# Kernel tuning notes

Measured on AMD Instinct MI355X. Metric: run time of the kernel, lower is better.

The kernel has to match this reference:

```python
import jax, jax.numpy as jnp
import numpy as np

MODES = (16, 16)

def setup_inputs() -> dict:
    key = jax.random.key(0)
    ks = jax.random.split(key, 8)
    B, Cin, Cout, H, W = 16, 64, 64, 128, 128
    scale = 1.0 / (Cin * Cout)
    return {
        "x": jax.random.normal(ks[0], (B, Cin, H, W), jnp.float32),
        "t_emb": jax.random.normal(ks[1], (B, 512), jnp.float32),
        "weight_real": jax.random.normal(ks[2], (Cin, Cout, *MODES), jnp.float32) * 2 * scale - scale,
        "weight_imag": jax.random.normal(ks[3], (Cin, Cout, *MODES), jnp.float32) * 2 * scale - scale,
        "bypass_w": jax.random.normal(ks[4], (Cout, Cin), jnp.float32) * 0.05,
        "bypass_b": jax.random.normal(ks[5], (Cout,), jnp.float32) * 0.05,
        "temb_w": jax.random.normal(ks[6], (Cin, 512), jnp.float32) * 0.02,
        "temb_b": jax.random.normal(ks[7], (Cin,), jnp.float32) * 0.02,
    }

def reference(x, t_emb, weight_real, weight_imag, bypass_w, bypass_b, temb_w, temb_b):
    mk, ml = MODES
    H, W = x.shape[-2:]
    xf = x.astype(jnp.float32)
    # truncated spectral conv: rfft2 (ortho), keep low-mode corner only
    x_fft = jnp.fft.rfftn(xf, axes=(-2, -1), norm="ortho")[:, :, :mk, :ml]
    weight = weight_real + 1j * weight_imag  # [i, o, k, l]
    out_fft = jnp.einsum("bikl,iokl->bokl", x_fft, weight)
    x_spec = jnp.fft.irfftn(out_fft, s=(H, W), axes=(-2, -1), norm="ortho")
    # 1x1 conv bypass
    byp = jnp.einsum("bihw,oi->bohw", xf, bypass_w) + bypass_b[None, :, None, None]
    out = jax.nn.gelu(x_spec + byp, approximate=False)
    # temb fusion: x + Linear(silu(temb))[:, :, None, None]
    silu_t = t_emb * jax.nn.sigmoid(t_emb)
    proj = silu_t @ temb_w.T + temb_b  # [B, C]
    out = out + proj[:, :, None, None]
    return out
```

## Files before the change

kernel.cpp:

```cpp
#include <hip/hip_runtime.h>
#include <cmath>

#define TWO_PI_128 0.04908738521234052f

typedef __attribute__((ext_vector_type(8))) short bf16x8;
typedef __attribute__((ext_vector_type(4))) float f32x4;

__device__ inline unsigned short f2bf(float v) {
  unsigned u = __float_as_uint(v);
  unsigned r = (u + 0x7FFFu + ((u >> 16) & 1u)) >> 16;
  return (unsigned short)r;
}

__global__ __launch_bounds__(256) void proj_kernel(
    const float* __restrict__ t_emb, const float* __restrict__ temb_w,
    const float* __restrict__ temb_b, float* __restrict__ proj) {
  __shared__ float s_silu[512];
  __shared__ float s_part[64][4];
  const int b = blockIdx.x;
  const int t = threadIdx.x;
  for (int j = t; j < 512; j += 256) {
    float v = t_emb[b * 512 + j];
    s_silu[j] = v / (1.f + __expf(-v));
  }
  __syncthreads();
  const int o = t >> 2, part = t & 3;
  const float* wrow = temb_w + o * 512 + part * 128;
  const float* srow = s_silu + part * 128;
  float acc = 0.f;
#pragma unroll 8
  for (int j = 0; j < 128; ++j) acc = fmaf(srow[j], wrow[j], acc);
  s_part[o][part] = acc;
  __syncthreads();
  if (part == 0) {
    proj[b * 64 + o] =
        s_part[o][0] + s_part[o][1] + s_part[o][2] + s_part[o][3] + temb_b[o];
  }
}

__global__ __launch_bounds__(256) void wtrans_kernel(
    const float* __restrict__ wr, const float* __restrict__ wi,
    float* __restrict__ wt_r, float* __restrict__ wt_i) {
  __shared__ float tile[32][33];
  const float* src = blockIdx.z ? wi : wr;
  float* dst = blockIdx.z ? wt_i : wt_r;
  const int kl0 = blockIdx.x * 32, io0 = blockIdx.y * 32;
  const int ty = threadIdx.x >> 3, tx = threadIdx.x & 7;
  float4 v = *(const float4*)(src + (size_t)(io0 + ty) * 256 + kl0 + 4 * tx);
  tile[ty][4 * tx + 0] = v.x;
  tile[ty][4 * tx + 1] = v.y;
  tile[ty][4 * tx + 2] = v.z;
  tile[ty][4 * tx + 3] = v.w;
  __syncthreads();
  float4 o;
  o.x = tile[4 * tx + 0][ty];
  o.y = tile[4 * tx + 1][ty];
  o.z = tile[4 * tx + 2][ty];
  o.w = tile[4 * tx + 3][ty];
  *(float4*)(dst + (size_t)(kl0 + ty) * 4096 + io0 + 4 * tx) = o;
}

__global__ __launch_bounds__(256) void fwd_dft_kernel(
    const float* __restrict__ x, float* __restrict__ xfr_t,
    float* __restrict__ xfi_t) {
  __shared__ unsigned short s_x1[32 * 136];
  __shared__ float s_red[8 * 256];
  const int t = threadIdx.x;
  const int plane = blockIdx.x;
  const int wv = t >> 6, lane = t & 63, l15 = lane & 15, quad = lane >> 4;

  union U8 {
    bf16x8 v;
    unsigned short u[8];
  };

  float dC, dS;
  sincosf(TWO_PI_128 * (float)l15, &dS, &dC);

  U8 a_re[4], a_im[4];
#pragma unroll
  for (int ks = 0; ks < 4; ++ks) {
    const int w0 = ks * 32 + quad * 8;
    float c, s;
    sincosf(TWO_PI_128 * (float)((l15 * w0) & 127), &s, &c);
#pragma unroll
    for (int j = 0; j < 8; ++j) {
      a_re[ks].u[j] = f2bf(c);
      a_im[ks].u[j] = f2bf(-s);
      float nc = c * dC - s * dS;
      s = s * dC + c * dS;
      c = nc;
    }
  }

  const float* xp = x + (size_t)plane * 16384;
  f32x4 acc[2][2];
#pragma unroll
  for (int mt = 0; mt < 2; ++mt)
#pragma unroll
    for (int nt = 0; nt < 2; ++nt) acc[mt][nt] = (f32x4){0.f, 0.f, 0.f, 0.f};

#pragma unroll
  for (int ks = 0; ks < 4; ++ks) {
#pragma unroll
    for (int nt = 0; nt < 2; ++nt) {
      const float* src =
          xp + (size_t)((wv * 2 + nt) * 16 + l15) * 128 + ks * 32 + quad * 8;
      float4 v0 = *(const float4*)src;
      float4 v1 = *(const float4*)(src + 4);
      U8 bx;
      bx.u[0] = f2bf(v0.x);
      bx.u[1] = f2bf(v0.y);
      bx.u[2] = f2bf(v0.z);
      bx.u[3] = f2bf(v0.w);
      bx.u[4] = f2bf(v1.x);
      bx.u[5] = f2bf(v1.y);
      bx.u[6] = f2bf(v1.z);
      bx.u[7] = f2bf(v1.w);
      acc[0][nt] = __builtin_amdgcn_mfma_f32_16x16x32_bf16(a_re[ks].v, bx.v,
                                                           acc[0][nt], 0, 0, 0);
      acc[1][nt] = __builtin_amdgcn_mfma_f32_16x16x32_bf16(a_im[ks].v, bx.v,
                                                           acc[1][nt], 0, 0, 0);
    }
  }

#pragma unroll
  for (int mt = 0; mt < 2; ++mt)
#pragma unroll
    for (int nt = 0; nt < 2; ++nt)
#pragma unroll
      for (int r = 0; r < 4; ++r)
        s_x1[(mt * 16 + quad * 4 + r) * 136 + (wv * 2 + nt) * 16 + l15] =
            f2bf(acc[mt][nt][r]);
  __syncthreads();

  f32x4 accre = (f32x4){0.f, 0.f, 0.f, 0.f};
  f32x4 accim = (f32x4){0.f, 0.f, 0.f, 0.f};
#pragma unroll
  for (int kl2 = 0; kl2 < 2; ++kl2) {
    const int ks2 = wv * 2 + kl2;
    const int hb = (ks2 & 3) * 32 + quad * 8;
    const int imh = ks2 >> 2;
    float c, s;
    sincosf(TWO_PI_128 * (float)((l15 * hb) & 127), &s, &c);
    U8 ar, ai;
#pragma unroll
    for (int j = 0; j < 8; ++j) {
      if (!imh) {
        ar.u[j] = f2bf(c);
        ai.u[j] = f2bf(-s);
      } else {
        ar.u[j] = f2bf(s);
        ai.u[j] = f2bf(c);
      }
      float nc = c * dC - s * dS;
      s = s * dC + c * dS;
      c = nc;
    }
    bf16x8 bfrag = *(const bf16x8*)(s_x1 + (imh * 16 + l15) * 136 + hb);
    accre =
        __builtin_amdgcn_mfma_f32_16x16x32_bf16(ar.v, bfrag, accre, 0, 0, 0);
    accim =
        __builtin_amdgcn_mfma_f32_16x16x32_bf16(ai.v, bfrag, accim, 0, 0, 0);
  }
  *(f32x4*)(s_red + (wv * 2) * 256 + lane * 4) = accre;
  *(f32x4*)(s_red + (wv * 2 + 1) * 256 + lane * 4) = accim;
  __syncthreads();

  const float re = s_red[t] + s_red[512 + t] + s_red[1024 + t] + s_red[1536 + t];
  const float im =
      s_red[256 + t] + s_red[768 + t] + s_red[1280 + t] + s_red[1792 + t];
  const int k = (t >> 6) * 4 + (t & 3), l = (t >> 2) & 15;
  xfr_t[(size_t)(k * 16 + l) * 1024 + plane] = re * 0.0078125f;
  xfi_t[(size_t)(k * 16 + l) * 1024 + plane] = im * 0.0078125f;
}

__global__ __launch_bounds__(256) void modemix_kernel(
    const float* __restrict__ xfr_t, const float* __restrict__ xfi_t,
    const float* __restrict__ wt_r, const float* __restrict__ wt_i,
    float* __restrict__ ofr, float* __restrict__ ofi) {
  __shared__ float s_xr[1024], s_xi[1024];
  __shared__ float s_wr[4096], s_wi[4096];
  const int kl = blockIdx.x;
  const int t = threadIdx.x;
  ((float4*)s_xr)[t] = ((const float4*)(xfr_t + (size_t)kl * 1024))[t];
  ((float4*)s_xi)[t] = ((const float4*)(xfi_t + (size_t)kl * 1024))[t];
  const float4* wrp = (const float4*)(wt_r + (size_t)kl * 4096);
  const float4* wip = (const float4*)(wt_i + (size_t)kl * 4096);
#pragma unroll
  for (int j = 0; j < 4; ++j) {
    ((float4*)s_wr)[t + 256 * j] = wrp[t + 256 * j];
    ((float4*)s_wi)[t + 256 * j] = wip[t + 256 * j];
  }
  __syncthreads();
  const int b0 = t >> 6;
  const int o = t & 63;
  float accr[4] = {0.f, 0.f, 0.f, 0.f};
  float acci[4] = {0.f, 0.f, 0.f, 0.f};
  for (int i = 0; i < 64; ++i) {
    float wrv = s_wr[i * 64 + o], wiv = s_wi[i * 64 + o];
#pragma unroll
    for (int j = 0; j < 4; ++j) {
      int b = b0 + 4 * j;
      float xr = s_xr[b * 64 + i], xi = s_xi[b * 64 + i];
      accr[j] = fmaf(xr, wrv, accr[j]);
      accr[j] = fmaf(-xi, wiv, accr[j]);
      acci[j] = fmaf(xr, wiv, acci[j]);
      acci[j] = fmaf(xi, wrv, acci[j]);
    }
  }
#pragma unroll
  for (int j = 0; j < 4; ++j) {
    int b = b0 + 4 * j;
    ofr[(size_t)(b * 64 + o) * 256 + kl] = accr[j];
    ofi[(size_t)(b * 64 + o) * 256 + kl] = acci[j];
  }
}

__global__ __launch_bounds__(256) void invh_kernel(
    const float* __restrict__ ofr, const float* __restrict__ ofi,
    uint4* __restrict__ Ybf) {
  __shared__ float s_fr[16 * 260], s_fi[16 * 260];
  __shared__ float2 s_tw[128];
  const int t = threadIdx.x;
  const int bid = blockIdx.x;
  const int b = bid >> 5, og = (bid >> 3) & 3, hg = bid & 7;
  if (t < 128) {
    float sv, cv;
    sincosf(TWO_PI_128 * (float)t, &sv, &cv);
    s_tw[t] = make_float2(cv, sv);
  }
#pragma unroll 4
  for (int pp = 0; pp < 16; ++pp) {
    s_fr[pp * 260 + t] = ofr[(size_t)(b * 64 + og * 16 + pp) * 256 + t];
    s_fi[pp * 260 + t] = ofi[(size_t)(b * 64 + og * 16 + pp) * 256 + t];
  }
  __syncthreads();
  const int ol = t & 15, hl = t >> 4;
  const int h = hg * 16 + hl;
  float yr[16], yi[16];
#pragma unroll
  for (int l = 0; l < 16; ++l) {
    yr[l] = 0.f;
    yi[l] = 0.f;
  }
  const float* FR = s_fr + ol * 260;
  const float* FI = s_fi + ol * 260;
  const float2 tw = s_tw[h];
  float ck = 1.f, sk = 0.f;
#pragma unroll 4
  for (int k = 0; k < 16; ++k) {
#pragma unroll
    for (int q = 0; q < 4; ++q) {
      float4 fr = *(const float4*)(FR + k * 16 + 4 * q);
      float4 fi = *(const float4*)(FI + k * 16 + 4 * q);
      int l = 4 * q;
      yr[l + 0] = fmaf(fr.x, ck, yr[l + 0]);
      yr[l + 0] = fmaf(-fi.x, sk, yr[l + 0]);
      yi[l + 0] = fmaf(fi.x, ck, yi[l + 0]);
      yi[l + 0] = fmaf(fr.x, sk, yi[l + 0]);
      yr[l + 1] = fmaf(fr.y, ck, yr[l + 1]);
      yr[l + 1] = fmaf(-fi.y, sk, yr[l + 1]);
      yi[l + 1] = fmaf(fi.y, ck, yi[l + 1]);
      yi[l + 1] = fmaf(fr.y, sk, yi[l + 1]);
      yr[l + 2] = fmaf(fr.z, ck, yr[l + 2]);
      yr[l + 2] = fmaf(-fi.z, sk, yr[l + 2]);
      yi[l + 2] = fmaf(fi.z, ck, yi[l + 2]);
      yi[l + 2] = fmaf(fr.z, sk, yi[l + 2]);
      yr[l + 3] = fmaf(fr.w, ck, yr[l + 3]);
      yr[l + 3] = fmaf(-fi.w, sk, yr[l + 3]);
      yi[l + 3] = fmaf(fi.w, ck, yi[l + 3]);
      yi[l + 3] = fmaf(fr.w, sk, yi[l + 3]);
    }
    float tt = sk * tw.y, uu = ck * tw.y;
    ck = fmaf(ck, tw.x, -tt);
    sk = fmaf(sk, tw.x, uu);
  }
  unsigned int u[16];
  {
    float sc[16];
    sc[0] = 0.0078125f;
#pragma unroll
    for (int l = 1; l < 16; ++l) sc[l] = 0.015625f;
#pragma unroll
    for (int j = 0; j < 8; ++j) {
      u[j] = (unsigned)f2bf(yr[2 * j] * sc[2 * j]) |
             ((unsigned)f2bf(yr[2 * j + 1] * sc[2 * j + 1]) << 16);
      u[8 + j] = (unsigned)f2bf(yi[2 * j] * sc[2 * j]) |
                 ((unsigned)f2bf(yi[2 * j + 1] * sc[2 * j + 1]) << 16);
    }
  }
  uint4* dst = Ybf + ((size_t)(b * 128 + h) * 64 + og * 16 + ol) * 4;
  dst[0] = make_uint4(u[0], u[1], u[2], u[3]);
  dst[1] = make_uint4(u[4], u[5], u[6], u[7]);
  dst[2] = make_uint4(u[8], u[9], u[10], u[11]);
  dst[3] = make_uint4(u[12], u[13], u[14], u[15]);
}

__global__ __launch_bounds__(256) void final_kernel(
    const float* __restrict__ x, const float* __restrict__ bw,
    const float* __restrict__ bb, const float* __restrict__ proj,
    const uint4* __restrict__ Ybf, float* __restrict__ out) {
#define AR 104
  __shared__ unsigned short s_A[64 * AR];
  __shared__ float s_bb[64];
  __shared__ float s_pb[64];
  const int h = blockIdx.x, b = blockIdx.y, t = threadIdx.x;

  if (t < 64)
    s_bb[t] = bb[t];
  else if (t < 128)
    s_pb[t - 64] = proj[b * 64 + (t - 64)];

  {
    const int o = t >> 2, q = t & 3;
    const float4* src = (const float4*)(bw + o * 64 + q * 16);
    unsigned int u[8];
#pragma unroll
    for (int m = 0; m < 4; ++m) {
      float4 v = src[m];
      u[2 * m] = (unsigned)f2bf(v.x) | ((unsigned)f2bf(v.y) << 16);
      u[2 * m + 1] = (unsigned)f2bf(v.z) | ((unsigned)f2bf(v.w) << 16);
    }
    uint4* dst = (uint4*)(s_A + o * AR + q * 16);
    dst[0] = make_uint4(u[0], u[1], u[2], u[3]);
    dst[1] = make_uint4(u[4], u[5], u[6], u[7]);
  }
  {
    const int o = t >> 2, q = t & 3;
    uint4 v = Ybf[((size_t)(b * 128 + h) * 64 + o) * 4 + q];
    *(uint4*)(s_A + o * AR + 64 + q * 8) = v;
  }
  __syncthreads();

  const int wv = t >> 6, lane = t & 63;
  const int l15 = lane & 15, quad = lane >> 4;
  const int n0w = wv * 32;

  f32x4 acc[4][2];
#pragma unroll
  for (int mt = 0; mt < 4; ++mt) {
    f32x4 bv = *(const f32x4*)(s_bb + mt * 16 + quad * 4);
    acc[mt][0] = bv;
    acc[mt][1] = bv;
  }

  const float* xrow = x + (size_t)b * 1048576 + (size_t)h * 128 + n0w + l15;
#pragma unroll
  for (int ks = 0; ks < 64; ks += 32) {
    union {
      bf16x8 v;
      unsigned short u[8];
    } bx[2];
#pragma unroll
    for (int nt = 0; nt < 2; ++nt) {
      float xv[8];
#pragma unroll
      for (int j = 0; j < 8; ++j)
        xv[j] = xrow[(size_t)(ks + quad * 8 + j) * 16384 + nt * 16];
#pragma unroll
      for (int j = 0; j < 8; ++j) bx[nt].u[j] = f2bf(xv[j]);
    }
#pragma unroll
    for (int mt = 0; mt < 4; ++mt) {
      bf16x8 a = *(const bf16x8*)(s_A + (mt * 16 + l15) * AR + ks + quad * 8);
      acc[mt][0] = __builtin_amdgcn_mfma_f32_16x16x32_bf16(a, bx[0].v,
                                                           acc[mt][0], 0, 0, 0);
      acc[mt][1] = __builtin_amdgcn_mfma_f32_16x16x32_bf16(a, bx[1].v,
                                                           acc[mt][1], 0, 0, 0);
    }
  }

  {
    const int lbase = (quad & 1) * 8;
    const bool iscos = (quad < 2);
    union {
      bf16x8 v;
      unsigned short u[8];
    } bs[2];
#pragma unroll
    for (int nt = 0; nt < 2; ++nt) {
      const int wn = n0w + nt * 16 + l15;
      float st, ct, ss, cc;
      sincosf(TWO_PI_128 * (float)wn, &st, &ct);
      sincosf(TWO_PI_128 * (float)(wn * lbase), &ss, &cc);
#pragma unroll
      for (int j = 0; j < 8; ++j) {
        bs[nt].u[j] = f2bf(iscos ? cc : -ss);
        float nc = cc * ct - ss * st;
        ss = ss * ct + cc * st;
        cc = nc;
      }
    }
#pragma unroll
    for (int mt = 0; mt < 4; ++mt) {
      bf16x8 a = *(const bf16x8*)(s_A + (mt * 16 + l15) * AR + 64 + quad * 8);
      acc[mt][0] = __builtin_amdgcn_mfma_f32_16x16x32_bf16(a, bs[0].v,
                                                           acc[mt][0], 0, 0, 0);
      acc[mt][1] = __builtin_amdgcn_mfma_f32_16x16x32_bf16(a, bs[1].v,
                                                           acc[mt][1], 0, 0, 0);
    }
  }

#pragma unroll
  for (int mt = 0; mt < 4; ++mt) {
    f32x4 pv = *(const f32x4*)(s_pb + mt * 16 + quad * 4);
#pragma unroll
    for (int nt = 0; nt < 2; ++nt) {
      const int wcol = n0w + nt * 16 + l15;
#pragma unroll
      for (int r = 0; r < 4; ++r) {
        const int o = mt * 16 + quad * 4 + r;
        float v = acc[mt][nt][r];
        float g = fmaf(0.5f * v, 1.f + erff(v * 0.70710678f), pv[r]);
        out[((size_t)(b * 64 + o) * 128 + h) * 128 + wcol] = g;
      }
    }
  }
#undef AR
}

extern "C" void kernel_launch(void* const* d_in, const int* in_sizes, int n_in,
                              void* d_out, int out_size, void* d_ws,
                              size_t ws_size, hipStream_t stream) {
  (void)in_sizes;
  (void)n_in;
  (void)out_size;
  (void)ws_size;
  const float* x = (const float*)d_in[0];
  const float* t_emb = (const float*)d_in[1];
  const float* wr = (const float*)d_in[2];
  const float* wi = (const float*)d_in[3];
  const float* bw = (const float*)d_in[4];
  const float* bb = (const float*)d_in[5];
  const float* tw = (const float*)d_in[6];
  const float* tb = (const float*)d_in[7];
  float* out = (float*)d_out;

  char* ws = (char*)d_ws;
  float* proj = (float*)(ws);
  float* ofr = (float*)(ws + ((size_t)1 << 20));
  float* ofi = (float*)(ws + ((size_t)2 << 20));
  float* xfr_t = (float*)(ws + ((size_t)3 << 20));
  float* xfi_t = (float*)(ws + ((size_t)4 << 20));
  float* wt_r = (float*)(ws + ((size_t)5 << 20));
  float* wt_i = (float*)(ws + ((size_t)9 << 20));
  uint4* Ybf = (uint4*)(ws + ((size_t)3 << 20));

  proj_kernel<<<16, 256, 0, stream>>>(t_emb, tw, tb, proj);
  wtrans_kernel<<<dim3(8, 128, 2), 256, 0, stream>>>(wr, wi, wt_r, wt_i);
  fwd_dft_kernel<<<1024, 256, 0, stream>>>(x, xfr_t, xfi_t);
  modemix_kernel<<<256, 256, 0, stream>>>(xfr_t, xfi_t, wt_r, wt_i, ofr, ofi);
  invh_kernel<<<512, 256, 0, stream>>>(ofr, ofi, Ybf);
  final_kernel<<<dim3(128, 16), 256, 0, stream>>>(x, bw, bb, proj, Ybf, out);
}
```

Before: 184.6 us.

## Precompute DFT twiddle tables, drop weight transpose, bf16 mode outputs, tanh GELU

Twiddle fragments for the forward DFT and the final kernel's inverse-W stage are now built once by an extra block in a merged setup kernel and loaded from global memory, where before every block recomputed them with sincos. The separate weight-transpose kernel is removed: modemix reads the original weights strided, handles two modes per block, and writes bf16-packed outputs that invh unpacks. The exact erf GELU is replaced by the tanh approximation. The changes reduce launches, trig work and intermediate traffic, but add strided weight reads, extra bf16 rounding and approximation error in GELU.

Result: slower. 194.2 us (+5.2%).

```diff
diff --git a/kernel.cpp b/kernel.cpp
--- a/kernel.cpp
+++ b/kernel.cpp
@@ -11,14 +11,105 @@
   unsigned r = (u + 0x7FFFu + ((u >> 16) & 1u)) >> 16;
   return (unsigned short)r;
 }
-
-__global__ __launch_bounds__(256) void proj_kernel(
+__device__ inline float bf2f(unsigned short s) {
+  return __uint_as_float(((unsigned)s) << 16);
+}
+__device__ inline unsigned pack2(float a, float b) {
+  return (unsigned)f2bf(a) | ((unsigned)f2bf(b) << 16);
+}
+__device__ inline float gelu_fast(float v) {
+  float z = 0.7978845608f * fmaf(0.044715f * v, v * v, v);
+  float e = __expf(2.f * z);
+  float th = 1.f - 2.f / (e + 1.f);
+  return 0.5f * v * (1.f + th);
+}
+
+__global__ __launch_bounds__(256) void setup_kernel(
     const float* __restrict__ t_emb, const float* __restrict__ temb_w,
-    const float* __restrict__ temb_b, float* __restrict__ proj) {
+    const float* __restrict__ temb_b, float* __restrict__ proj,
+    uint4* __restrict__ ftab1, uint4* __restrict__ ftab2,
+    uint4* __restrict__ stab) {
+  const int t = threadIdx.x;
+  if (blockIdx.x == 0) {
+    const int lane = t & 63, l15 = lane & 15, quad = lane >> 4;
+    const int wv = t >> 6;
+    union U8 {
+      uint4 q;
+      unsigned short u[8];
+    };
+    float dC, dS;
+    sincosf(TWO_PI_128 * (float)l15, &dS, &dC);
+    if (t < 64) {
+#pragma unroll
+      for (int ks = 0; ks < 4; ++ks) {
+        const int w0 = ks * 32 + quad * 8;
+        float c, s;
+        sincosf(TWO_PI_128 * (float)((l15 * w0) & 127), &s, &c);
+        U8 re, im;
+#pragma unroll
+        for (int j = 0; j < 8; ++j) {
+          re.u[j] = f2bf(c);
+          im.u[j] = f2bf(-s);
+          float nc = c * dC - s * dS;
+          s = s * dC + c * dS;
+          c = nc;
+        }
+        ftab1[lane * 8 + ks] = re.q;
+        ftab1[lane * 8 + 4 + ks] = im.q;
+      }
+    }
+    {
+#pragma unroll
+      for (int kl2 = 0; kl2 < 2; ++kl2) {
+        const int ks2 = wv * 2 + kl2;
+        const int hb = (ks2 & 3) * 32 + quad * 8;
+        const int imh = ks2 >> 2;
+        float c, s;
+        sincosf(TWO_PI_128 * (float)((l15 * hb) & 127), &s, &c);
+        U8 ar, ai;
+#pragma unroll
+        for (int j = 0; j < 8; ++j) {
+          if (!imh) {
+            ar.u[j] = f2bf(c);
+            ai.u[j] = f2bf(-s);
+          } else {
+            ar.u[j] = f2bf(s);
+            ai.u[j] = f2bf(c);
+          }
+          float nc = c * dC - s * dS;
+          s = s * dC + c * dS;
+          c = nc;
+        }
+        ftab2[t * 4 + kl2 * 2] = ar.q;
+        ftab2[t * 4 + kl2 * 2 + 1] = ai.q;
+      }
+    }
+    {
+      const int n0w = wv * 32;
+      const int lbase = (quad & 1) * 8;
+      const bool iscos = (quad < 2);
+#pragma unroll
+      for (int nt = 0; nt < 2; ++nt) {
+        const int wn = n0w + nt * 16 + l15;
+        float st, ct, ss, cc;
+        sincosf(TWO_PI_128 * (float)wn, &st, &ct);
+        sincosf(TWO_PI_128 * (float)(wn * lbase), &ss, &cc);
+        U8 bs;
+#pragma unroll
+        for (int j = 0; j < 8; ++j) {
+          bs.u[j] = f2bf(iscos ? cc : -ss);
+          float nc = cc * ct - ss * st;
+          ss = ss * ct + cc * st;
+          cc = nc;
+        }
+        stab[t * 2 + nt] = bs.q;
+      }
+    }
+    return;
+  }
   __shared__ float s_silu[512];
   __shared__ float s_part[64][4];
-  const int b = blockIdx.x;
-  const int t = threadIdx.x;
+  const int b = blockIdx.x - 1;
   for (int j = t; j < 512; j += 256) {
     float v = t_emb[b * 512 + j];
     s_silu[j] = v / (1.f + __expf(-v));
@@ -38,30 +129,9 @@
   }
 }
 
-__global__ __launch_bounds__(256) void wtrans_kernel(
-    const float* __restrict__ wr, const float* __restrict__ wi,
-    float* __restrict__ wt_r, float* __restrict__ wt_i) {
-  __shared__ float tile[32][33];
-  const float* src = blockIdx.z ? wi : wr;
-  float* dst = blockIdx.z ? wt_i : wt_r;
-  const int kl0 = blockIdx.x * 32, io0 = blockIdx.y * 32;
-  const int ty = threadIdx.x >> 3, tx = threadIdx.x & 7;
-  float4 v = *(const float4*)(src + (size_t)(io0 + ty) * 256 + kl0 + 4 * tx);
-  tile[ty][4 * tx + 0] = v.x;
-  tile[ty][4 * tx + 1] = v.y;
-  tile[ty][4 * tx + 2] = v.z;
-  tile[ty][4 * tx + 3] = v.w;
-  __syncthreads();
-  float4 o;
-  o.x = tile[4 * tx + 0][ty];
-  o.y = tile[4 * tx + 1][ty];
-  o.z = tile[4 * tx + 2][ty];
-  o.w = tile[4 * tx + 3][ty];
-  *(float4*)(dst + (size_t)(kl0 + ty) * 4096 + io0 + 4 * tx) = o;
-}
-
 __global__ __launch_bounds__(256) void fwd_dft_kernel(
-    const float* __restrict__ x, float* __restrict__ xfr_t,
+    const float* __restrict__ x, const uint4* __restrict__ ftab1,
+    const uint4* __restrict__ ftab2, float* __restrict__ xfr_t,
     float* __restrict__ xfi_t) {
   __shared__ unsigned short s_x1[32 * 136];
   __shared__ float s_red[8 * 256];
@@ -70,27 +140,16 @@
   const int wv = t >> 6, lane = t & 63, l15 = lane & 15, quad = lane >> 4;
 
   union U8 {
+    uint4 q;
     bf16x8 v;
     unsigned short u[8];
   };
 
-  float dC, dS;
-  sincosf(TWO_PI_128 * (float)l15, &dS, &dC);
-
   U8 a_re[4], a_im[4];
 #pragma unroll
   for (int ks = 0; ks < 4; ++ks) {
-    const int w0 = ks * 32 + quad * 8;
-    float c, s;
-    sincosf(TWO_PI_128 * (float)((l15 * w0) & 127), &s, &c);
-#pragma unroll
-    for (int j = 0; j < 8; ++j) {
-      a_re[ks].u[j] = f2bf(c);
-      a_im[ks].u[j] = f2bf(-s);
-      float nc = c * dC - s * dS;
-      s = s * dC + c * dS;
-      c = nc;
-    }
+    a_re[ks].q = ftab1[lane * 8 + ks];
+    a_im[ks].q = ftab1[lane * 8 + 4 + ks];
   }
 
   const float* xp = x + (size_t)plane * 16384;
@@ -141,22 +200,9 @@
     const int ks2 = wv * 2 + kl2;
     const int hb = (ks2 & 3) * 32 + quad * 8;
     const int imh = ks2 >> 2;
-    float c, s;
-    sincosf(TWO_PI_128 * (float)((l15 * hb) & 127), &s, &c);
     U8 ar, ai;
-#pragma unroll
-    for (int j = 0; j < 8; ++j) {
-      if (!imh) {
-        ar.u[j] = f2bf(c);
-        ai.u[j] = f2bf(-s);
-      } else {
-        ar.u[j] = f2bf(s);
-        ai.u[j] = f2bf(c);
-      }
-      float nc = c * dC - s * dS;
-      s = s * dC + c * dS;
-      c = nc;
-    }
+    ar.q = ftab2[t * 4 + kl2 * 2];
+    ai.q = ftab2[t * 4 + kl2 * 2 + 1];
     bf16x8 bfrag = *(const bf16x8*)(s_x1 + (imh * 16 + l15) * 136 + hb);
     accre =
         __builtin_amdgcn_mfma_f32_16x16x32_bf16(ar.v, bfrag, accre, 0, 0, 0);
@@ -177,48 +223,69 @@
 
 __global__ __launch_bounds__(256) void modemix_kernel(
     const float* __restrict__ xfr_t, const float* __restrict__ xfi_t,
-    const float* __restrict__ wt_r, const float* __restrict__ wt_i,
-    float* __restrict__ ofr, float* __restrict__ ofi) {
-  __shared__ float s_xr[1024], s_xi[1024];
-  __shared__ float s_wr[4096], s_wi[4096];
-  const int kl = blockIdx.x;
+    const float* __restrict__ wr, const float* __restrict__ wi,
+    unsigned* __restrict__ ofr_bf, unsigned* __restrict__ ofi_bf) {
+  __shared__ float s_x[4][1024];
+  __shared__ float s_w[4][4096];
+  const int klp = blockIdx.x, kl0 = klp * 2;
   const int t = threadIdx.x;
-  ((float4*)s_xr)[t] = ((const float4*)(xfr_t + (size_t)kl * 1024))[t];
-  ((float4*)s_xi)[t] = ((const float4*)(xfi_t + (size_t)kl * 1024))[t];
-  const float4* wrp = (const float4*)(wt_r + (size_t)kl * 4096);
-  const float4* wip = (const float4*)(wt_i + (size_t)kl * 4096);
+  {
+    const float4* sr = (const float4*)(xfr_t + (size_t)kl0 * 1024);
+    const float4* si = (const float4*)(xfi_t + (size_t)kl0 * 1024);
+    ((float4*)&s_x[0][0])[t] = sr[t];
+    ((float4*)&s_x[0][0])[t + 256] = sr[t + 256];
+    ((float4*)&s_x[2][0])[t] = si[t];
+    ((float4*)&s_x[2][0])[t + 256] = si[t + 256];
+  }
+#pragma unroll 4
+  for (int j = 0; j < 16; ++j) {
+    int io = t + 256 * j;
+    float2 vr = *(const float2*)(wr + (size_t)io * 256 + kl0);
+    float2 vi = *(const float2*)(wi + (size_t)io * 256 + kl0);
+    s_w[0][io] = vr.x;
+    s_w[1][io] = vr.y;
+    s_w[2][io] = vi.x;
+    s_w[3][io] = vi.y;
+  }
+  __syncthreads();
+  const int b0 = t >> 6, o = t & 63;
+  float rr[2][4], ri[2][4];
+#pragma unroll
+  for (int ks = 0; ks < 2; ++ks) {
+    float accr[4] = {0.f, 0.f, 0.f, 0.f};
+    float acci[4] = {0.f, 0.f, 0.f, 0.f};
+    const float* xr = s_x[ks];
+    const float* xi = s_x[2 + ks];
+    const float* wrp = s_w[ks];
+    const float* wip = s_w[2 + ks];
+    for (int i = 0; i < 64; ++i) {
+      float wrv = wrp[i * 64 + o], wiv = wip[i * 64 + o];
+#pragma unroll
+      for (int j = 0; j < 4; ++j) {
+        int b = b0 + 4 * j;
+        float xrv = xr[b * 64 + i], xiv = xi[b * 64 + i];
+        accr[j] = fmaf(xrv, wrv, accr[j]);
+        accr[j] = fmaf(-xiv, wiv, accr[j]);
+        acci[j] = fmaf(xrv, wiv, acci[j]);
+        acci[j] = fmaf(xiv, wrv, acci[j]);
+      }
+    }
+#pragma unroll
+    for (int j = 0; j < 4; ++j) {
+      rr[ks][j] = accr[j];
+      ri[ks][j] = acci[j];
+    }
+  }
 #pragma unroll
   for (int j = 0; j < 4; ++j) {
-    ((float4*)s_wr)[t + 256 * j] = wrp[t + 256 * j];
-    ((float4*)s_wi)[t + 256 * j] = wip[t + 256 * j];
-  }
-  __syncthreads();
-  const int b0 = t >> 6;
-  const int o = t & 63;
-  float accr[4] = {0.f, 0.f, 0.f, 0.f};
-  float acci[4] = {0.f, 0.f, 0.f, 0.f};
-  for (int i = 0; i < 64; ++i) {
-    float wrv = s_wr[i * 64 + o], wiv = s_wi[i * 64 + o];
-#pragma unroll
-    for (int j = 0; j < 4; ++j) {
-      int b = b0 + 4 * j;
-      float xr = s_xr[b * 64 + i], xi = s_xi[b * 64 + i];
-      accr[j] = fmaf(xr, wrv, accr[j]);
-      accr[j] = fmaf(-xi, wiv, accr[j]);
-      acci[j] = fmaf(xr, wiv, acci[j]);
-      acci[j] = fmaf(xi, wrv, acci[j]);
-    }
-  }
-#pragma unroll
-  for (int j = 0; j < 4; ++j) {
-    int b = b0 + 4 * j;
-    ofr[(size_t)(b * 64 + o) * 256 + kl] = accr[j];
-    ofi[(size_t)(b * 64 + o) * 256 + kl] = acci[j];
+    int plane = (b0 + 4 * j) * 64 + o;
+    ofr_bf[(size_t)plane * 128 + klp] = pack2(rr[0][j], rr[1][j]);
+    ofi_bf[(size_t)plane * 128 + klp] = pack2(ri[0][j], ri[1][j]);
   }
 }
 
 __global__ __launch_bounds__(256) void invh_kernel(
-    const float* __restrict__ ofr, const float* __restrict__ ofi,
+    const unsigned* __restrict__ ofr_bf, const unsigned* __restrict__ ofi_bf,
     uint4* __restrict__ Ybf) {
   __shared__ float s_fr[16 * 260], s_fi[16 * 260];
   __shared__ float2 s_tw[128];
@@ -231,9 +298,15 @@
     s_tw[t] = make_float2(cv, sv);
   }
 #pragma unroll 4
-  for (int pp = 0; pp < 16; ++pp) {
-    s_fr[pp * 260 + t] = ofr[(size_t)(b * 64 + og * 16 + pp) * 256 + t];
-    s_fi[pp * 260 + t] = ofi[(size_t)(b * 64 + og * 16 + pp) * 256 + t];
+  for (int pp = 0; pp < 8; ++pp) {
+    const int row = pp * 2 + (t >> 7);
+    const int col = t & 127;
+    unsigned ur = ofr_bf[(size_t)(b * 64 + og * 16 + row) * 128 + col];
+    unsigned ui = ofi_bf[(size_t)(b * 64 + og * 16 + row) * 128 + col];
+    s_fr[row * 260 + 2 * col] = bf2f((unsigned short)(ur & 0xFFFFu));
+    s_fr[row * 260 + 2 * col + 1] = bf2f((unsigned short)(ur >> 16));
+    s_fi[row * 260 + 2 * col] = bf2f((unsigned short)(ui & 0xFFFFu));
+    s_fi[row * 260 + 2 * col + 1] = bf2f((unsigned short)(ui >> 16));
   }
   __syncthreads();
   const int ol = t & 15, hl = t >> 4;
@@ -277,18 +350,13 @@
     sk = fmaf(sk, tw.x, uu);
   }
   unsigned int u[16];
-  {
-    float sc[16];
-    sc[0] = 0.0078125f;
-#pragma unroll
-    for (int l = 1; l < 16; ++l) sc[l] = 0.015625f;
-#pragma unroll
-    for (int j = 0; j < 8; ++j) {
-      u[j] = (unsigned)f2bf(yr[2 * j] * sc[2 * j]) |
-             ((unsigned)f2bf(yr[2 * j + 1] * sc[2 * j + 1]) << 16);
-      u[8 + j] = (unsigned)f2bf(yi[2 * j] * sc[2 * j]) |
-                 ((unsigned)f2bf(yi[2 * j + 1] * sc[2 * j + 1]) << 16);
-    }
+#pragma unroll
+  for (int j = 0; j < 8; ++j) {
+    float s0 = (2 * j == 0) ? 0.0078125f : 0.015625f;
+    u[j] = (unsigned)f2bf(yr[2 * j] * s0) |
+           ((unsigned)f2bf(yr[2 * j + 1] * 0.015625f) << 16);
+    u[8 + j] = (unsigned)f2bf(yi[2 * j] * s0) |
+               ((unsigned)f2bf(yi[2 * j + 1] * 0.015625f) << 16);
   }
   uint4* dst = Ybf + ((size_t)(b * 128 + h) * 64 + og * 16 + ol) * 4;
   dst[0] = make_uint4(u[0], u[1], u[2], u[3]);
@@ -300,7 +368,8 @@
 __global__ __launch_bounds__(256) void final_kernel(
     const float* __restrict__ x, const float* __restrict__ bw,
     const float* __restrict__ bb, const float* __restrict__ proj,
-    const uint4* __restrict__ Ybf, float* __restrict__ out) {
+    const uint4* __restrict__ Ybf, const uint4* __restrict__ stab,
+    float* __restrict__ out) {
 #define AR 104
   __shared__ unsigned short s_A[64 * AR];
   __shared__ float s_bb[64];
@@ -372,32 +441,18 @@
   }
 
   {
-    const int lbase = (quad & 1) * 8;
-    const bool iscos = (quad < 2);
     union {
+      uint4 q;
       bf16x8 v;
-      unsigned short u[8];
-    } bs[2];
-#pragma unroll
-    for (int nt = 0; nt < 2; ++nt) {
-      const int wn = n0w + nt * 16 + l15;
-      float st, ct, ss, cc;
-      sincosf(TWO_PI_128 * (float)wn, &st, &ct);
-      sincosf(TWO_PI_128 * (float)(wn * lbase), &ss, &cc);
-#pragma unroll
-      for (int j = 0; j < 8; ++j) {
-        bs[nt].u[j] = f2bf(iscos ? cc : -ss);
-        float nc = cc * ct - ss * st;
-        ss = ss * ct + cc * st;
-        cc = nc;
-      }
-    }
+    } bs0, bs1;
+    bs0.q = stab[t * 2];
+    bs1.q = stab[t * 2 + 1];
 #pragma unroll
     for (int mt = 0; mt < 4; ++mt) {
       bf16x8 a = *(const bf16x8*)(s_A + (mt * 16 + l15) * AR + 64 + quad * 8);
-      acc[mt][0] = __builtin_amdgcn_mfma_f32_16x16x32_bf16(a, bs[0].v,
+      acc[mt][0] = __builtin_amdgcn_mfma_f32_16x16x32_bf16(a, bs0.v,
                                                            acc[mt][0], 0, 0, 0);
-      acc[mt][1] = __builtin_amdgcn_mfma_f32_16x16x32_bf16(a, bs[1].v,
+      acc[mt][1] = __builtin_amdgcn_mfma_f32_16x16x32_bf16(a, bs1.v,
                                                            acc[mt][1], 0, 0, 0);
     }
   }
@@ -412,8 +467,8 @@
       for (int r = 0; r < 4; ++r) {
         const int o = mt * 16 + quad * 4 + r;
         float v = acc[mt][nt][r];
-        float g = fmaf(0.5f * v, 1.f + erff(v * 0.70710678f), pv[r]);
-        out[((size_t)(b * 64 + o) * 128 + h) * 128 + wcol] = g;
+        out[((size_t)(b * 64 + o) * 128 + h) * 128 + wcol] =
+            gelu_fast(v) + pv[r];
       }
     }
   }
@@ -439,18 +494,19 @@
 
   char* ws = (char*)d_ws;
   float* proj = (float*)(ws);
-  float* ofr = (float*)(ws + ((size_t)1 << 20));
-  float* ofi = (float*)(ws + ((size_t)2 << 20));
+  uint4* ftab1 = (uint4*)(ws + (64 << 10));
+  uint4* ftab2 = (uint4*)(ws + (96 << 10));
+  uint4* stab = (uint4*)(ws + (128 << 10));
+  unsigned* ofr_bf = (unsigned*)(ws + ((size_t)1 << 20));
+  unsigned* ofi_bf = (unsigned*)(ws + ((size_t)2 << 20));
   float* xfr_t = (float*)(ws + ((size_t)3 << 20));
   float* xfi_t = (float*)(ws + ((size_t)4 << 20));
-  float* wt_r = (float*)(ws + ((size_t)5 << 20));
-  float* wt_i = (float*)(ws + ((size_t)9 << 20));
-  uint4* Ybf = (uint4*)(ws + ((size_t)3 << 20));
-
-  proj_kernel<<<16, 256, 0, stream>>>(t_emb, tw, tb, proj);
-  wtrans_kernel<<<dim3(8, 128, 2), 256, 0, stream>>>(wr, wi, wt_r, wt_i);
-  fwd_dft_kernel<<<1024, 256, 0, stream>>>(x, xfr_t, xfi_t);
-  modemix_kernel<<<256, 256, 0, stream>>>(xfr_t, xfi_t, wt_r, wt_i, ofr, ofi);
-  invh_kernel<<<512, 256, 0, stream>>>(ofr, ofi, Ybf);
-  final_kernel<<<dim3(128, 16), 256, 0, stream>>>(x, bw, bb, proj, Ybf, out);
-}
+  uint4* Ybf = (uint4*)(ws + ((size_t)5 << 20));
+
+  setup_kernel<<<17, 256, 0, stream>>>(t_emb, tw, tb, proj, ftab1, ftab2, stab);
+  fwd_dft_kernel<<<1024, 256, 0, stream>>>(x, ftab1, ftab2, xfr_t, xfi_t);
+  modemix_kernel<<<128, 256, 0, stream>>>(xfr_t, xfi_t, wr, wi, ofr_bf, ofi_bf);
+  invh_kernel<<<512, 256, 0, stream>>>(ofr_bf, ofi_bf, Ybf);
+  final_kernel<<<dim3(128, 16), 256, 0, stream>>>(x, bw, bb, proj, Ybf, stab,
+                                                  out);
+}
```
